# Kernel tuning notes

Measured on AMD Instinct MI355X. Metric: run time of the kernel, lower is better.

The kernel has to match this reference:

```python
import jax, jax.numpy as jnp
import numpy as np

H = 1024          # hidden_size
NH = 16           # num_heads = hidden_size // head_dim
DK = 64           # head_dim (key)
DV = 64           # head_v_dim
VDIM = 1024       # value_dim
DECAY_LR, GATE_LR, A_LR, V_LR = 64, 160, 64, 64
W_SCALE = -0.6065306597126334  # -exp(-0.5)
GN_EPS = 64 * 1e-5             # head_dim * norm_eps


def _lora(x, A, B, b, act):
    h = x @ A.T
    if act is not None:
        h = act(h)
    y = h @ B.T
    return y if b is None else y + b


def setup_inputs() -> dict:
    key = jax.random.key(0)
    ks = iter(jax.random.split(key, 40))
    def n(shape, s=0.02):
        return jax.random.normal(next(ks), shape, dtype=jnp.float32) * s
    inp = {
        'hidden_states': jax.random.normal(next(ks), (8, 2048, H), jnp.float32),
        'v_first': jax.random.normal(next(ks), (8, 2048, VDIM), jnp.float32),
        'x_r': n((1, 1, H), 0.5), 'x_w': n((1, 1, H), 0.5), 'x_k': n((1, 1, H), 0.5),
        'x_v': n((1, 1, H), 0.5), 'x_a': n((1, 1, H), 0.5), 'x_g': n((1, 1, H), 0.5),
        'k_k': 0.71 + n((H,), 0.05),
        'k_a': 1.02 + n((H,), 0.05),
        'r_k': -0.04 + n((NH, DK), 0.05),
        'W_r': n((H, H)), 'W_k': n((H, H)), 'W_v': n((VDIM, H)), 'W_o': n((H, VDIM)),
        'w_lora_A': n((DECAY_LR, H)), 'w_lora_B': n((H, DECAY_LR)), 'w_lora_b': n((H,), 0.5) - 4.0,
        'a_lora_A': n((A_LR, H)), 'a_lora_B': n((H, A_LR)), 'a_lora_b': n((H,), 0.1),
        'v_lora_A': n((V_LR, H)), 'v_lora_B': n((VDIM, V_LR)), 'v_lora_b': 0.73 + n((VDIM,), 0.1),
        'g_lora_A': n((GATE_LR, H)), 'g_lora_B': n((VDIM, GATE_LR)),
        'gn_w': jnp.ones((VDIM,), jnp.float32), 'gn_b': jnp.zeros((VDIM,), jnp.float32),
    }
    return inp


def reference(hidden_states, v_first, x_r, x_w, x_k, x_v, x_a, x_g, k_k, k_a, r_k,
              W_r, W_k, W_v, W_o, w_lora_A, w_lora_B, w_lora_b,
              a_lora_A, a_lora_B, a_lora_b, v_lora_A, v_lora_B, v_lora_b,
              g_lora_A, g_lora_B, gn_w, gn_b):
    x = hidden_states
    B_, T, _ = x.shape
    # token shift: delta[t] = x[t-1] - x[t], x[-1] = 0
    shifted = jnp.pad(x, ((0, 0), (1, 0), (0, 0)))[:, :T]
    delta = shifted - x
    xr = x + delta * x_r; xw = x + delta * x_w; xk = x + delta * x_k
    xv = x + delta * x_v; xa = x + delta * x_a; xg = x + delta * x_g

    r = xr @ W_r.T
    w = W_SCALE * jax.nn.sigmoid(_lora(xw, w_lora_A, w_lora_B, w_lora_b, jnp.tanh))  # log-decay in (-e^-0.5, 0)
    k = xk @ W_k.T
    v = xv @ W_v.T
    v = v + (v_first - v) * jax.nn.sigmoid(_lora(xv, v_lora_A, v_lora_B, v_lora_b, None))  # layer_idx != 0
    a = jax.nn.sigmoid(_lora(xa, a_lora_A, a_lora_B, a_lora_b, None))
    g = _lora(xg, g_lora_A, g_lora_B, None, jax.nn.sigmoid)

    kk = (k * k_k).reshape(B_, T, NH, DK)
    kk = kk / jnp.maximum(jnp.linalg.norm(kk, axis=-1, keepdims=True), 1e-12)  # l2 norm per head
    k = k * (1.0 + (a - 1.0) * k_a)

    rh = r.reshape(B_, T, NH, DK)
    wh = w.reshape(B_, T, NH, DK)
    kh = k.reshape(B_, T, NH, DK)
    vh = v.reshape(B_, T, NH, DV)
    ah = -kk                               # delta-rule 'a' (removal direction)
    bh = kk * a.reshape(B_, T, NH, DK)     # delta-rule 'b' (write direction)

    def step(S, inputs):
        # S: [B, H, DK, DV]; inputs each [B, H, D]
        r_t, w_t, k_t, v_t, a_t, b_t = inputs
        sa = jnp.einsum('bhk,bhkv->bhv', a_t, S)
        S = S * jnp.exp(w_t)[..., None] \
            + jnp.einsum('bhk,bhv->bhkv', b_t, sa) \
            + jnp.einsum('bhk,bhv->bhkv', k_t, v_t)
        o_t = jnp.einsum('bhk,bhkv->bhv', r_t, S)
        return S, o_t

    seq = tuple(jnp.moveaxis(t, 1, 0) for t in (rh, wh, kh, vh, ah, bh))  # [T,B,H,D]
    S0 = jnp.zeros((B_, NH, DK, DV), dtype=x.dtype)
    _, o = jax.lax.scan(step, S0, seq)
    o = jnp.moveaxis(o, 0, 1)  # [B, T, NH, DV]

    # GroupNorm with num_groups = num_heads over value_dim channels == per-head LayerNorm (no per-head affine)
    mu = o.mean(-1, keepdims=True)
    var = o.var(-1, keepdims=True)
    on = ((o - mu) / jnp.sqrt(var + GN_EPS)).reshape(B_, T, VDIM) * gn_w + gn_b

    bonus = ((rh * kh * r_k).sum(-1, keepdims=True) * vh).reshape(B_, T, VDIM)
    out = ((on + bonus) * g) @ W_o.T
    return out
```

## Files before the change

kernel.cpp:

```cpp
#include <hip/hip_runtime.h>
#include <hip/hip_bf16.h>


#define DEVI __device__ __forceinline__

constexpr int TSEQ = 2048;
constexpr int HID  = 1024;
constexpr int BTOT = 16384;
constexpr int CCH  = 32;
constexpr int NCH  = TSEQ / CCH;
constexpr int L4N  = 352;
constexpr float W_SCALE = -0.6065306597126334f;
constexpr float GN_EPS  = 6.4e-4f;

using s16x8  = __attribute__((ext_vector_type(8))) short;
using f32x4v = __attribute__((ext_vector_type(4))) float;

DEVI float4 ld4(const float* p) { return *reinterpret_cast<const float4*>(p); }
DEVI void   st4(float* p, float4 v) { *reinterpret_cast<float4*>(p) = v; }
DEVI float  sigf(float x) { return 1.0f / (1.0f + __expf(-x)); }
DEVI unsigned short bfr(float f) {
    unsigned int u = __float_as_uint(f);
    return (unsigned short)((u + 0x7fffu + ((u >> 16) & 1u)) >> 16);
}
DEVI float bff(unsigned short s) { return __uint_as_float(((unsigned int)s) << 16); }
DEVI unsigned int pk2(float lo, float hi) {
    return ((unsigned int)bfr(hi) << 16) | (unsigned int)bfr(lo);
}
DEVI void up8(uint4 u, float* f) {
    f[0]=bff((unsigned short)(u.x & 0xffffu)); f[1]=bff((unsigned short)(u.x >> 16));
    f[2]=bff((unsigned short)(u.y & 0xffffu)); f[3]=bff((unsigned short)(u.y >> 16));
    f[4]=bff((unsigned short)(u.z & 0xffffu)); f[5]=bff((unsigned short)(u.z >> 16));
    f[6]=bff((unsigned short)(u.w & 0xffffu)); f[7]=bff((unsigned short)(u.w >> 16));
}
DEVI f32x4v MF(s16x8 a, s16x8 b, f32x4v c) {
    return __builtin_amdgcn_mfma_f32_16x16x32_bf16(a, b, c, 0, 0, 0);
}
DEVI void gl16(const void* g, void* l) {
    __builtin_amdgcn_global_load_lds(
        (const __attribute__((address_space(1))) unsigned int*)g,
        (__attribute__((address_space(3))) unsigned int*)l, 16, 0, 0);
}
DEVI void gl4(const void* g, void* l) {
    __builtin_amdgcn_global_load_lds(
        (const __attribute__((address_space(1))) unsigned int*)g,
        (__attribute__((address_space(3))) unsigned int*)l, 4, 0, 0);
}

struct CastArgs {
    const float* src[12];
    unsigned short* dst[12];
    int start4[13];
};
__global__ __launch_bounds__(256) void cast_all_kernel(CastArgs a) {
    int i4 = blockIdx.x * 256 + threadIdx.x;
    if (i4 >= a.start4[12]) return;
    int seg = 0;
#pragma unroll
    for (int s = 1; s < 12; s++) seg += (i4 >= a.start4[s]) ? 1 : 0;
    int off = (i4 - a.start4[seg]) * 4;
    float4 v = ld4(a.src[seg] + off);
    ushort4 o; o.x = bfr(v.x); o.y = bfr(v.y); o.z = bfr(v.z); o.w = bfr(v.w);
    *reinterpret_cast<ushort4*>(a.dst[seg] + off) = o;
}

__global__ __launch_bounds__(256) void proj3_kernel(
        const float* __restrict__ x,
        const float* __restrict__ cr, const float* __restrict__ ck,
        const float* __restrict__ cv,
        const unsigned short* __restrict__ Wr, const unsigned short* __restrict__ Wk,
        const unsigned short* __restrict__ Wv,
        unsigned short* __restrict__ Ro, unsigned short* __restrict__ Ko,
        unsigned short* __restrict__ Vo) {
    __shared__ __align__(16) unsigned short As[3][64 * 32];
    __shared__ __align__(16) unsigned short Bs[3][128 * 32];
    const int tid = threadIdx.x;
    const int w = tid >> 6, l = tid & 63;
    const int bm = blockIdx.x * 64, bn = blockIdx.y * 128;
    const int wm = w >> 1, wn = w & 1;
    const int lr = l & 15, lq = l >> 4, lk = lq * 8;

    f32x4v acc[3][2][4];
#pragma unroll
    for (int p = 0; p < 3; p++)
#pragma unroll
        for (int i = 0; i < 2; i++)
#pragma unroll
            for (int j = 0; j < 4; j++)
#pragma unroll
                for (int q = 0; q < 4; q++) acc[p][i][j][q] = 0.f;

    const float* cvs[3] = {cr, ck, cv};
    const unsigned short* Ws[3] = {Wr, Wk, Wv};

    for (int k0 = 0; k0 < HID; k0 += 32) {
        {
            const int row = tid >> 2, kp = (tid & 3) * 8;
            const int gr = bm + row;
            const float* xp = x + (size_t)gr * HID + k0 + kp;
            float4 x0 = ld4(xp), x1 = ld4(xp + 4);
            float4 p0 = make_float4(0.f, 0.f, 0.f, 0.f), p1 = p0;
            if ((gr & (TSEQ - 1)) != 0) { p0 = ld4(xp - HID); p1 = ld4(xp - HID + 4); }
            float xb[8] = {x0.x, x0.y, x0.z, x0.w, x1.x, x1.y, x1.z, x1.w};
            float dx[8] = {p0.x - x0.x, p0.y - x0.y, p0.z - x0.z, p0.w - x0.w,
                           p1.x - x1.x, p1.y - x1.y, p1.z - x1.z, p1.w - x1.w};
#pragma unroll
            for (int p = 0; p < 3; p++) {
                float4 c0 = ld4(cvs[p] + k0 + kp), c1 = ld4(cvs[p] + k0 + kp + 4);
                float cc[8] = {c0.x, c0.y, c0.z, c0.w, c1.x, c1.y, c1.z, c1.w};
                uint4 u;
                u.x = pk2(fmaf(dx[0], cc[0], xb[0]), fmaf(dx[1], cc[1], xb[1]));
                u.y = pk2(fmaf(dx[2], cc[2], xb[2]), fmaf(dx[3], cc[3], xb[3]));
                u.z = pk2(fmaf(dx[4], cc[4], xb[4]), fmaf(dx[5], cc[5], xb[5]));
                u.w = pk2(fmaf(dx[6], cc[6], xb[6]), fmaf(dx[7], cc[7], xb[7]));
                *reinterpret_cast<uint4*>(&As[p][row * 32 + kp]) = u;
            }
        }
#pragma unroll
        for (int p = 0; p < 3; p++)
#pragma unroll
            for (int c = 0; c < 2; c++) {
                int idx = c * 256 + tid;
                int rw = idx >> 2, kp2 = (idx & 3) * 8;
                gl16(Ws[p] + (size_t)(bn + rw) * HID + k0 + kp2,
                     &Bs[p][c * 2048 + w * 512]);
            }
        __syncthreads();
#pragma unroll
        for (int p = 0; p < 3; p++) {
            s16x8 af[2], bf4[4];
#pragma unroll
            for (int i = 0; i < 2; i++)
                af[i] = *reinterpret_cast<const s16x8*>(
                    &As[p][(wm * 32 + i * 16 + lr) * 32 + lk]);
#pragma unroll
            for (int j = 0; j < 4; j++)
                bf4[j] = *reinterpret_cast<const s16x8*>(
                    &Bs[p][(wn * 64 + j * 16 + lr) * 32 + lk]);
#pragma unroll
            for (int i = 0; i < 2; i++)
#pragma unroll
                for (int j = 0; j < 4; j++)
                    acc[p][i][j] = MF(af[i], bf4[j], acc[p][i][j]);
        }
        __syncthreads();
    }

    unsigned short* dsts[3] = {Ro, Ko, Vo};
#pragma unroll
    for (int p = 0; p < 3; p++)
#pragma unroll
        for (int i = 0; i < 2; i++)
#pragma unroll
            for (int j = 0; j < 4; j++)
#pragma unroll
                for (int q = 0; q < 4; q++) {
                    const int grow = bm + wm * 32 + i * 16 + lq * 4 + q;
                    const int gcol = bn + wn * 64 + j * 16 + lr;
                    dsts[p][(size_t)grow * HID + gcol] = bfr(acc[p][i][j][q]);
                }
}

__global__ __launch_bounds__(256) void lora4_kernel(
        const float* __restrict__ x,
        const float* __restrict__ cv_, const float* __restrict__ cw_,
        const float* __restrict__ ca_, const float* __restrict__ cg_,
        const unsigned short* __restrict__ LW, unsigned short* __restrict__ H1) {
    __shared__ __align__(16) unsigned short As[4][64 * 32];
    __shared__ __align__(16) unsigned short Bs[L4N * 32];
    const int tid = threadIdx.x;
    const int w = tid >> 6, l = tid & 63;
    const int lr = l & 15, lq = l >> 4, lk = lq * 8;
    const int bm = blockIdx.x * 64;
    const float* cvs[4] = {cv_, cw_, ca_, cg_};

    f32x4v acc[22];
#pragma unroll
    for (int j = 0; j < 22; j++)
#pragma unroll
        for (int q = 0; q < 4; q++) acc[j][q] = 0.f;

    for (int k0 = 0; k0 < HID; k0 += 32) {
        {
            const int row = tid >> 2, kp = (tid & 3) * 8;
            const int gr = bm + row;
            const float* xp = x + (size_t)gr * HID + k0 + kp;
            float4 x0 = ld4(xp), x1 = ld4(xp + 4);
            float4 p0 = make_float4(0.f, 0.f, 0.f, 0.f), p1 = p0;
            if ((gr & (TSEQ - 1)) != 0) { p0 = ld4(xp - HID); p1 = ld4(xp - HID + 4); }
            float xb[8] = {x0.x, x0.y, x0.z, x0.w, x1.x, x1.y, x1.z, x1.w};
            float dx[8] = {p0.x - x0.x, p0.y - x0.y, p0.z - x0.z, p0.w - x0.w,
                           p1.x - x1.x, p1.y - x1.y, p1.z - x1.z, p1.w - x1.w};
#pragma unroll
            for (int p = 0; p < 4; p++) {
                float4 c0 = ld4(cvs[p] + k0 + kp), c1 = ld4(cvs[p] + k0 + kp + 4);
                float cc[8] = {c0.x, c0.y, c0.z, c0.w, c1.x, c1.y, c1.z, c1.w};
                uint4 u;
                u.x = pk2(fmaf(dx[0], cc[0], xb[0]), fmaf(dx[1], cc[1], xb[1]));
                u.y = pk2(fmaf(dx[2], cc[2], xb[2]), fmaf(dx[3], cc[3], xb[3]));
                u.z = pk2(fmaf(dx[4], cc[4], xb[4]), fmaf(dx[5], cc[5], xb[5]));
                u.w = pk2(fmaf(dx[6], cc[6], xb[6]), fmaf(dx[7], cc[7], xb[7]));
                *reinterpret_cast<uint4*>(&As[p][row * 32 + kp]) = u;
            }
        }
#pragma unroll
        for (int c = 0; c < 6; c++) {
            int idx = c * 256 + tid;
            if (idx < L4N * 4) {
                gl16(LW + (size_t)(idx >> 2) * HID + (idx & 3) * 8 + k0,
                     (char*)&Bs[0] + (c * 256 + w * 64) * 16);
            }
        }
        __syncthreads();
        s16x8 af[4];
#pragma unroll
        for (int p = 0; p < 4; p++)
            af[p] = *reinterpret_cast<const s16x8*>(&As[p][(w * 16 + lr) * 32 + lk]);
#pragma unroll
        for (int j = 0; j < 22; j++) {
            const int grp = (j < 4) ? 0 : (j < 8) ? 1 : (j < 12) ? 2 : 3;
            s16x8 bf = *reinterpret_cast<const s16x8*>(&Bs[(j * 16 + lr) * 32 + lk]);
            acc[j] = MF(af[grp], bf, acc[j]);
        }
        __syncthreads();
    }

#pragma unroll
    for (int j = 0; j < 22; j++)
#pragma unroll
        for (int q = 0; q < 4; q++) {
            const int grow = bm + w * 16 + lq * 4 + q;
            const int gcol = j * 16 + lr;
            float d = acc[j][q];
            if (j >= 4 && j < 8) d = tanhf(d);
            else if (j >= 12) d = sigf(d);
            H1[(size_t)grow * L4N + gcol] = bfr(d);
        }
}

__global__ __launch_bounds__(256) void stage2_kernel(
        const unsigned short* __restrict__ H1,
        const unsigned short* __restrict__ vB16, const unsigned short* __restrict__ wB16,
        const unsigned short* __restrict__ aB16,
        const float* __restrict__ vb, const float* __restrict__ wb,
        const float* __restrict__ ab,
        unsigned short* __restrict__ Vout, unsigned short* __restrict__ Wout,
        unsigned short* __restrict__ Aout,
        const unsigned short* __restrict__ aux1, const float* __restrict__ aux2) {
    const int z = blockIdx.z;
    const unsigned short* Bw = (z == 0) ? vB16 : (z == 1) ? wB16 : aB16;
    const float* bias = (z == 0) ? vb : (z == 1) ? wb : ab;
    unsigned short* Cout = (z == 0) ? Vout : (z == 1) ? Wout : Aout;
    const int aoff = z * 64;
    __shared__ __align__(16) unsigned short As[128 * 32];
    __shared__ __align__(16) unsigned short Bs[128 * 32];
    const int tid = threadIdx.x;
    const int w = tid >> 6, l = tid & 63;
    const int bm = blockIdx.x * 128, bn = blockIdx.y * 128;
    const int wm = w >> 1, wn = w & 1;
    const int lr = l & 15, lk = (l >> 4) * 8;

    f32x4v acc[4][4];
#pragma unroll
    for (int i = 0; i < 4; i++)
#pragma unroll
        for (int j = 0; j < 4; j++)
#pragma unroll
            for (int q = 0; q < 4; q++) acc[i][j][q] = 0.f;

    for (int k0 = 0; k0 < 64; k0 += 32) {
#pragma unroll
        for (int c = 0; c < 2; c++) {
            int idx = c * 256 + tid;
            int row = idx >> 2, kp = (idx & 3) * 8;
            gl16(H1 + (size_t)(bm + row) * L4N + aoff + k0 + kp,
                 &As[c * 2048 + w * 512]);
        }
#pragma unroll
        for (int c = 0; c < 2; c++) {
            int idx = c * 256 + tid;
            int row = idx >> 2, kp = (idx & 3) * 8;
            gl16(Bw + (size_t)(bn + row) * 64 + k0 + kp, &Bs[c * 2048 + w * 512]);
        }
        __syncthreads();
        s16x8 afx[4], bfx[4];
#pragma unroll
        for (int i = 0; i < 4; i++)
            afx[i] = *reinterpret_cast<const s16x8*>(&As[(wm * 64 + i * 16 + lr) * 32 + lk]);
#pragma unroll
        for (int j = 0; j < 4; j++)
            bfx[j] = *reinterpret_cast<const s16x8*>(&Bs[(wn * 64 + j * 16 + lr) * 32 + lk]);
#pragma unroll
        for (int i = 0; i < 4; i++)
#pragma unroll
            for (int j = 0; j < 4; j++)
                acc[i][j] = MF(afx[i], bfx[j], acc[i][j]);
        __syncthreads();
    }

#pragma unroll
    for (int i = 0; i < 4; i++) {
        const int grow0 = bm + wm * 64 + i * 16 + (l >> 4) * 4;
#pragma unroll
        for (int j = 0; j < 4; j++) {
            const int gcol = bn + wn * 64 + j * 16 + lr;
            const float bsv = bias[gcol];
#pragma unroll
            for (int q = 0; q < 4; q++) {
                const int grow = grow0 + q;
                float d = acc[i][j][q];
                if (z == 0) {
                    float v0 = bff(aux1[(size_t)grow * HID + gcol]);
                    d = fmaf(aux2[(size_t)grow * HID + gcol] - v0, sigf(d + bsv), v0);
                } else if (z == 1) {
                    d = W_SCALE * sigf(d + bsv);
                } else {
                    d = sigf(d + bsv);
                }
                Cout[(size_t)grow * HID + gcol] = bfr(d);
            }
        }
    }
}

template<int BM, int BN, int MODE, bool OUTBF>
__global__ __launch_bounds__(256) void mgemm(
        const unsigned short* __restrict__ Ab, const unsigned short* __restrict__ Bw,
        void* Cout, int N, int K, int lda,
        const float* __restrict__ bias,
        const unsigned short* aux1, const float* __restrict__ aux2) {
    constexpr int BK = 32;
    constexpr int WM_ = (BN == 128) ? 2 : 4;
    constexpr int WN_ = (BN == 128) ? 2 : 1;
    constexpr int WTM = BM / WM_, WTN = BN / WN_;
    constexpr int MF_ = WTM / 16, NF = WTN / 16;
    constexpr int ACALLS = (BM * BK) / 2048;
    constexpr int BCALLS = (BN * BK) / 2048;
    __shared__ __align__(16) unsigned short As[BM * BK];
    __shared__ __align__(16) unsigned short Bs[BN * BK];
    const int tid = threadIdx.x;
    const int w = tid >> 6, l = tid & 63;
    const int bm = blockIdx.x * BM, bn = blockIdx.y * BN;
    const int wm = w / WN_, wn = w % WN_;
    const int lr = l & 15, lk = (l >> 4) * 8;

    f32x4v acc[MF_][NF];
#pragma unroll
    for (int i = 0; i < MF_; i++)
#pragma unroll
        for (int j = 0; j < NF; j++)
#pragma unroll
            for (int q = 0; q < 4; q++) acc[i][j][q] = 0.f;

    for (int k0 = 0; k0 < K; k0 += BK) {
#pragma unroll
        for (int c = 0; c < ACALLS; c++) {
            int idx = c * 256 + tid;
            int row = idx >> 2, kp = (idx & 3) * 8;
            gl16(Ab + (size_t)(bm + row) * lda + k0 + kp, &As[c * 2048 + w * 512]);
        }
#pragma unroll
        for (int c = 0; c < BCALLS; c++) {
            int idx = c * 256 + tid;
            int row = idx >> 2, kp = (idx & 3) * 8;
            int gc = bn + row; if (gc > N - 1) gc = N - 1;
            gl16(Bw + (size_t)gc * K + k0 + kp, &Bs[c * 2048 + w * 512]);
        }
        __syncthreads();
        s16x8 afx[MF_], bfx[NF];
#pragma unroll
        for (int i = 0; i < MF_; i++)
            afx[i] = *reinterpret_cast<const s16x8*>(&As[(wm * WTM + i * 16 + lr) * BK + lk]);
#pragma unroll
        for (int j = 0; j < NF; j++)
            bfx[j] = *reinterpret_cast<const s16x8*>(&Bs[(wn * WTN + j * 16 + lr) * BK + lk]);
#pragma unroll
        for (int i = 0; i < MF_; i++)
#pragma unroll
            for (int j = 0; j < NF; j++)
                acc[i][j] = __builtin_amdgcn_mfma_f32_16x16x32_bf16(
                    afx[i], bfx[j], acc[i][j], 0, 0, 0);
        __syncthreads();
    }

#pragma unroll
    for (int i = 0; i < MF_; i++) {
        const int grow0 = bm + wm * WTM + i * 16 + (l >> 4) * 4;
#pragma unroll
        for (int j = 0; j < NF; j++) {
            const int gcol = bn + wn * WTN + j * 16 + lr;
            if (gcol >= N) continue;
#pragma unroll
            for (int q = 0; q < 4; q++) {
                const int grow = grow0 + q;
                float d = acc[i][j][q];
                if (OUTBF) ((unsigned short*)Cout)[(size_t)grow * N + gcol] = bfr(d);
                else       ((float*)Cout)[(size_t)grow * N + gcol] = d;
            }
        }
    }
}

__global__ __launch_bounds__(64) void cprep_kernel(
        unsigned short* __restrict__ K16, unsigned short* __restrict__ A16,
        unsigned short* __restrict__ R16, unsigned short* __restrict__ KK16,
        const unsigned short* __restrict__ W16,
        const float* __restrict__ kkc, const float* __restrict__ kac,
        const float* __restrict__ rkw,
        float* __restrict__ SB, float* __restrict__ Ed,
        unsigned short* __restrict__ MvH, unsigned short* __restrict__ MvL) {
    __shared__ __align__(16) unsigned short sA[32][64], sB[32][64];
    __shared__ __align__(16) float Mab[32][36];
    const int bid = blockIdx.x;
    const int bh = bid >> 6, ch = bid & 63;
    const int bb = bh >> 4, hh = bh & 15;
    const int l = threadIdx.x;
    const int chn = hh * 64 + l;
    const float kkcv = kkc[chn], kacv = kac[chn], rkv = rkw[chn];
    size_t off = ((size_t)(bb * TSEQ) + ch * CCH) * HID + chn;
    float cw = 0.f, er = 1.f;
    for (int i = 0; i < CCH; i++, off += HID) {
        const float k = bff(K16[off]);
        const float a = bff(A16[off]);
        const float r = bff(R16[off]);
        const float wv = bff(W16[off]);
        const float kr = k * kkcv;
        float ss = kr * kr;
        ss += __shfl_xor(ss, 1);  ss += __shfl_xor(ss, 2);
        ss += __shfl_xor(ss, 4);  ss += __shfl_xor(ss, 8);
        ss += __shfl_xor(ss, 16); ss += __shfl_xor(ss, 32);
        const float inv = 1.0f / fmaxf(sqrtf(ss), 1e-12f);
        const float kk = kr * inv;
        const float b  = kk * a;
        const float kn = k * fmaf(a - 1.0f, kacv, 1.0f);
        float s3 = r * kn * rkv;
        s3 += __shfl_xor(s3, 1);  s3 += __shfl_xor(s3, 2);
        s3 += __shfl_xor(s3, 4);  s3 += __shfl_xor(s3, 8);
        s3 += __shfl_xor(s3, 16); s3 += __shfl_xor(s3, 32);
        if (l == 0) SB[(size_t)bh * TSEQ + ch * CCH + i] = s3;
        const float cwp = cw; cw += wv;
        const float ea = __expf(cwp), ei = __expf(-cw);
        er = __expf(cw);
        const unsigned short At = bfr(-kk * ea);
        const unsigned short Bt = bfr(b * ei);
        KK16[off] = At;
        A16[off]  = Bt;
        K16[off]  = bfr(kn * ei);
        R16[off]  = bfr(r * er);
        sA[i][l] = At; sB[i][l] = Bt;
    }
    Ed[((size_t)bh * NCH + ch) * 64 + l] = er;
    __syncthreads();
    const int lr = l & 15, lq = l >> 4;
    f32x4v z4; z4[0] = z4[1] = z4[2] = z4[3] = 0.f;
#pragma unroll
    for (int mi = 0; mi < 2; mi++)
#pragma unroll
        for (int ni = 0; ni < 2; ni++) {
            s16x8 a0 = *reinterpret_cast<const s16x8*>(&sA[mi * 16 + lr][lq * 8]);
            s16x8 a1 = *reinterpret_cast<const s16x8*>(&sA[mi * 16 + lr][32 + lq * 8]);
            s16x8 b0 = *reinterpret_cast<const s16x8*>(&sB[ni * 16 + lr][lq * 8]);
            s16x8 b1 = *reinterpret_cast<const s16x8*>(&sB[ni * 16 + lr][32 + lq * 8]);
            f32x4v m = MF(a1, b1, MF(a0, b0, z4));
#pragma unroll
            for (int q = 0; q < 4; q++) {
                int r = mi * 16 + lq * 4 + q, cc2 = ni * 16 + lr;
                Mab[r][cc2] = (cc2 < r) ? m[q] : 0.f;
            }
        }
    __syncthreads();
    const int j = l & 31;
    float m[32];
#pragma unroll
    for (int i = 0; i < 32; i++) m[i] = (i == j) ? 1.f : 0.f;
#pragma unroll
    for (int i = 1; i < 32; i++) {
        float p0 = 0.f, p1 = 0.f, p2 = 0.f, p3 = 0.f;
#pragma unroll
        for (int k4_ = 0; k4_ < 32; k4_ += 4) {
            if (k4_ >= i) break;
            float4 L4 = *reinterpret_cast<const float4*>(&Mab[i][k4_]);
            p0 = fmaf(L4.x, m[k4_ + 0], p0);
            if (k4_ + 1 < i) p1 = fmaf(L4.y, m[k4_ + 1], p1);
            if (k4_ + 2 < i) p2 = fmaf(L4.z, m[k4_ + 2], p2);
            if (k4_ + 3 < i) p3 = fmaf(L4.w, m[k4_ + 3], p3);
        }
        m[i] += (p0 + p1) + (p2 + p3);
    }
    if (l < 32) {
        unsigned short* dH = MvH + (size_t)(bh * NCH + ch) * 1024;
        unsigned short* dL = MvL + (size_t)(bh * NCH + ch) * 1024;
#pragma unroll
        for (int i = 0; i < 32; i++) {
            unsigned short h = bfr(m[i]);
            dH[i * 32 + j] = h;
            dL[i * 32 + j] = bfr(m[i] - bff(h));
        }
    }
}

__global__ __launch_bounds__(256) void recchunk_kernel(
        const unsigned short* __restrict__ AtG, const unsigned short* __restrict__ BtG,
        const unsigned short* __restrict__ KtG, const unsigned short* __restrict__ RtG,
        const unsigned short* __restrict__ V16, const float* __restrict__ Ed,
        const unsigned short* __restrict__ MvH, const unsigned short* __restrict__ MvL,
        unsigned short* __restrict__ Ob16) {
    __shared__ __align__(16) unsigned short stT[2][4][CCH][64];
    __shared__ __align__(16) unsigned short stMh[2][32][32], stMl[2][32][32];
    __shared__ __align__(16) unsigned short stV[2][CCH][16];
    __shared__ __align__(16) float stEd[2][64];
    __shared__ __align__(16) unsigned short Shi[16][74], Slo[16][74];
    __shared__ __align__(16) unsigned short BtT[64][42], KtT[64][42];
    __shared__ __align__(16) unsigned short VT[16][42];
    __shared__ __align__(16) unsigned short MakH[32][42], MakL[32][42];
    __shared__ __align__(16) unsigned short MrkH[32][42], MrkL[32][42];
    __shared__ __align__(16) unsigned short MrbH[32][42], MrbL[32][42];
    __shared__ __align__(16) unsigned short rhTH[16][42], rhTL[16][42];

    const int bid = blockIdx.x;
    const int vq = bid >> 7, bh = bid & 127;
    const int tid = threadIdx.x;
    const int w = tid >> 6, l = tid & 63;
    const int lr = l & 15, lq = l >> 4;
    const int bb = bh >> 4, hh = bh & 15;
    const size_t rowoff = ((size_t)bb * TSEQ) * HID + hh * 64;
    const int mi = w >> 1, ni = w & 1;

    const int r8 = l >> 3, ck = l & 7;
    const int swz8 = (ck ^ r8) * 8;

    auto STAGE = [&](int buf, int cn) {
        if (cn >= NCH) return;
        const size_t cb = rowoff + (size_t)(cn * CCH) * HID;
        const unsigned short* srcs[4] = {AtG, BtG, KtG, RtG};
        const unsigned short* T = srcs[w];
#pragma unroll
        for (int c = 0; c < 4; c++)
            gl16(T + cb + (size_t)(c * 8 + r8) * HID + swz8, &stT[buf][w][c * 8][0]);
        if (w == 0) {
            gl16(V16 + cb + (size_t)(l >> 1) * HID + vq * 16 + (l & 1) * 8,
                 &stV[buf][0][0]);
            gl4(Ed + ((size_t)bh * NCH + cn) * 64 + l, &stEd[buf][0]);
        } else if (w == 1) {
#pragma unroll
            for (int c = 0; c < 2; c++)
                gl16(MvH + (size_t)(bh * NCH + cn) * 1024 + c * 512 + l * 8,
                     (char*)&stMh[buf][0][0] + c * 1024);
        } else if (w == 2) {
#pragma unroll
            for (int c = 0; c < 2; c++)
                gl16(MvL + (size_t)(bh * NCH + cn) * 1024 + c * 512 + l * 8,
                     (char*)&stMl[buf][0][0] + c * 1024);
        }
    };

    for (int idx = tid; idx < 16 * 74; idx += 256) {
        ((unsigned short*)Shi)[idx] = 0;
        ((unsigned short*)Slo)[idx] = 0;
    }
    STAGE(0, 0);
    asm volatile("s_waitcnt vmcnt(0)" ::: "memory");
    __syncthreads();

    auto fragT = [&](int bf, int tn, int rbase, int kb) -> s16x8 {
        int row = rbase + lr;
        int chv = ((kb >> 3) + lq) ^ (row & 7);
        return *reinterpret_cast<const s16x8*>(
            (const char*)&stT[bf][tn][0][0] + row * 128 + chv * 16);
    };
    auto fragS = [&](const unsigned short (*Sx)[74], int kb) -> s16x8 {
        return *reinterpret_cast<const s16x8*>(&Sx[lr][kb + lq * 8]);
    };
    auto frag42 = [&](const unsigned short (*T)[42], int rbase) -> s16x8 {
        return *reinterpret_cast<const s16x8*>(&T[rbase + lr][lq * 8]);
    };

    f32x4v Sacc;
#pragma unroll
    for (int q = 0; q < 4; q++) Sacc[q] = 0.f;
    f32x4v z4; z4[0] = z4[1] = z4[2] = z4[3] = 0.f;

    int buf = 0;
    for (int c = 0; c < NCH; c++) {
        STAGE(buf ^ 1, c + 1);
        {
            const int tt = tid & 31, g8 = tid >> 5;
            const int ch = g8 ^ (tt & 7);
            uint4 bu = *reinterpret_cast<const uint4*>(&stT[buf][1][tt][ch * 8]);
            uint4 ku = *reinterpret_cast<const uint4*>(&stT[buf][2][tt][ch * 8]);
            unsigned int bw[4] = {bu.x, bu.y, bu.z, bu.w};
            unsigned int kw[4] = {ku.x, ku.y, ku.z, ku.w};
#pragma unroll
            for (int e = 0; e < 4; e++) {
                BtT[g8 * 8 + 2 * e][tt]     = (unsigned short)(bw[e] & 0xffffu);
                BtT[g8 * 8 + 2 * e + 1][tt] = (unsigned short)(bw[e] >> 16);
                KtT[g8 * 8 + 2 * e][tt]     = (unsigned short)(kw[e] & 0xffffu);
                KtT[g8 * 8 + 2 * e + 1][tt] = (unsigned short)(kw[e] >> 16);
            }
            if (g8 < 4) {
                ushort4 vu = *reinterpret_cast<const ushort4*>(&stV[buf][tt][g8 * 4]);
                VT[g8 * 4 + 0][tt] = vu.x; VT[g8 * 4 + 1][tt] = vu.y;
                VT[g8 * 4 + 2][tt] = vu.z; VT[g8 * 4 + 3][tt] = vu.w;
            }
        }
        s16x8 atm0 = fragT(buf, 0, mi * 16, 0), atm1 = fragT(buf, 0, mi * 16, 32);
        s16x8 rt0  = fragT(buf, 3, mi * 16, 0), rt1  = fragT(buf, 3, mi * 16, 32);
        s16x8 bt0  = fragT(buf, 1, ni * 16, 0), bt1  = fragT(buf, 1, ni * 16, 32);
        s16x8 kt0  = fragT(buf, 2, ni * 16, 0), kt1  = fragT(buf, 2, ni * 16, 32);
        f32x4v mak = MF(atm1, kt1, MF(atm0, kt0, z4));
        f32x4v mrk = MF(rt1, kt1, MF(rt0, kt0, z4));
        f32x4v mrb = MF(rt1, bt1, MF(rt0, bt0, z4));
        f32x4v oac = z4, rhT = z4;
        {
            s16x8 sh0 = fragS(Shi, 0), sh1 = fragS(Shi, 32);
            s16x8 sl0 = fragS(Slo, 0), sl1 = fragS(Slo, 32);
            if (ni == 0) {
                oac = MF(rt1, sl1, MF(rt0, sl0, MF(rt1, sh1, MF(rt0, sh0, z4))));
            } else {
                rhT = MF(sl1, atm1, MF(sl0, atm0, MF(sh1, atm1, MF(sh0, atm0, z4))));
            }
        }
#pragma unroll
        for (int q = 0; q < 4; q++) {
            const int r = mi * 16 + lq * 4 + q, cc = ni * 16 + lr;
            float vv = (cc < r) ? mak[q] : 0.f;
            unsigned short h = bfr(vv);
            MakH[r][cc] = h; MakL[r][cc] = bfr(vv - bff(h));
            vv = (cc <= r) ? mrk[q] : 0.f; h = bfr(vv);
            MrkH[r][cc] = h; MrkL[r][cc] = bfr(vv - bff(h));
            vv = (cc <= r) ? mrb[q] : 0.f; h = bfr(vv);
            MrbH[r][cc] = h; MrbL[r][cc] = bfr(vv - bff(h));
        }
        __syncthreads();
        {
            s16x8 vt0 = frag42(VT, 0);
            if (ni == 0) {
                oac = MF(frag42(MrkL, mi * 16), vt0,
                         MF(frag42(MrkH, mi * 16), vt0, oac));
            } else {
                rhT = MF(vt0, frag42(MakL, mi * 16),
                         MF(vt0, frag42(MakH, mi * 16), rhT));
#pragma unroll
                for (int q = 0; q < 4; q++) {
                    const int r = lq * 4 + q, cc = mi * 16 + lr;
                    unsigned short h = bfr(rhT[q]);
                    rhTH[r][cc] = h; rhTL[r][cc] = bfr(rhT[q] - bff(h));
                }
            }
        }
        __syncthreads();
        if (ni == 1) {
            s16x8 rh0 = frag42(rhTH, 0), rl0 = frag42(rhTL, 0);
            s16x8 mvh = *reinterpret_cast<const s16x8*>(&stMh[buf][mi * 16 + lr][lq * 8]);
            s16x8 mvl = *reinterpret_cast<const s16x8*>(&stMl[buf][mi * 16 + lr][lq * 8]);
            f32x4v sat = MF(rl0, mvh, MF(rh0, mvl, MF(rh0, mvh, z4)));
#pragma unroll
            for (int q = 0; q < 4; q++) {
                const int r = lq * 4 + q, cc = mi * 16 + lr;
                unsigned short h = bfr(sat[q]);
                MakH[r][cc] = h;
                MakL[r][cc] = bfr(sat[q] - bff(h));
            }
        }
        __syncthreads();
        {
            s16x8 sath = frag42(MakH, 0), satl = frag42(MakL, 0);
            if (ni == 0) {
                s16x8 rbh = frag42(MrbH, mi * 16), rbl = frag42(MrbL, mi * 16);
                oac = MF(rbl, sath, MF(rbh, satl, MF(rbh, sath, oac)));
#pragma unroll
                for (int q = 0; q < 4; q++) {
                    const int t = c * CCH + mi * 16 + lq * 4 + q;
                    Ob16[rowoff + (size_t)t * HID + vq * 16 + lr] = bfr(oac[q]);
                }
            }
            s16x8 btf = frag42(BtT, w * 16);
            s16x8 ktf = frag42(KtT, w * 16);
            s16x8 vta = frag42(VT, 0);
            const float ed = stEd[buf][w * 16 + lr];
            Sacc = MF(sath, btf, Sacc);
            Sacc = MF(satl, btf, Sacc);
            Sacc = MF(vta, ktf, Sacc);
#pragma unroll
            for (int q = 0; q < 4; q++) {
                Sacc[q] *= ed;
                unsigned short h = bfr(Sacc[q]);
                Shi[lq * 4 + q][w * 16 + lr] = h;
                Slo[lq * 4 + q][w * 16 + lr] = bfr(Sacc[q] - bff(h));
            }
        }
        asm volatile("s_waitcnt vmcnt(0)" ::: "memory");
        __syncthreads();
        buf ^= 1;
    }
}

__global__ __launch_bounds__(256) void stats_kernel(
        const unsigned short* __restrict__ O16, float* __restrict__ MS) {
    const int row = blockIdx.x;
    const int tid = threadIdx.x;
    const int c = tid * 4;
    ushort4 ou = *reinterpret_cast<const ushort4*>(O16 + (size_t)row * HID + c);
    float o[4] = {bff(ou.x), bff(ou.y), bff(ou.z), bff(ou.w)};
    float s1 = o[0] + o[1] + o[2] + o[3];
    float s2 = o[0]*o[0] + o[1]*o[1] + o[2]*o[2] + o[3]*o[3];
#pragma unroll
    for (int m = 1; m < 16; m <<= 1) {
        s1 += __shfl_xor(s1, m); s2 += __shfl_xor(s2, m);
    }
    if ((tid & 15) == 0) {
        const int hh = tid >> 4;
        const float mu = s1 * (1.0f / 64.0f);
        const float var = s2 * (1.0f / 64.0f) - mu * mu;
        float2 v; v.x = mu; v.y = rsqrtf(var + GN_EPS);
        *reinterpret_cast<float2*>(MS + (size_t)row * 32 + hh * 2) = v;
    }
}

__global__ __launch_bounds__(256) void wogemm_kernel(
        const unsigned short* __restrict__ O16, const unsigned short* __restrict__ V16,
        const unsigned short* __restrict__ G16, const float* __restrict__ SB,
        const float* __restrict__ MS, const float* __restrict__ gnw,
        const float* __restrict__ gnb, const unsigned short* __restrict__ Wo,
        float* __restrict__ out) {
    __shared__ __align__(16) unsigned short As[128 * 32];
    __shared__ __align__(16) unsigned short Bs[128 * 32];
    const int tid = threadIdx.x;
    const int w = tid >> 6, l = tid & 63;
    const int bm = blockIdx.x * 128, bn = blockIdx.y * 128;
    const int wm = w >> 1, wn = w & 1;
    const int lr = l & 15, lk = (l >> 4) * 8;

    f32x4v acc[4][4];
#pragma unroll
    for (int i = 0; i < 4; i++)
#pragma unroll
        for (int j = 0; j < 4; j++)
#pragma unroll
            for (int q = 0; q < 4; q++) acc[i][j][q] = 0.f;

    for (int k0 = 0; k0 < HID; k0 += 32) {
#pragma unroll
        for (int c = 0; c < 2; c++) {
            int idx = c * 256 + tid;
            int row = idx >> 2, kp = (idx & 3) * 8;
            const int gr = bm + row;
            const size_t rb = (size_t)gr * HID + k0 + kp;
            uint4 ou = *reinterpret_cast<const uint4*>(O16 + rb);
            uint4 vu = *reinterpret_cast<const uint4*>(V16 + rb);
            uint4 gu = *reinterpret_cast<const uint4*>(G16 + rb);
            float o8[8], v8[8], g8[8];
            up8(ou, o8); up8(vu, v8); up8(gu, g8);
            const int hh = (k0 + kp) >> 6;
            float2 ms = *reinterpret_cast<const float2*>(MS + (size_t)gr * 32 + hh * 2);
            const float s3 = SB[((size_t)(gr >> 11) * 16 + hh) * TSEQ + (gr & (TSEQ - 1))];
            float4 w0 = ld4(gnw + k0 + kp), w1 = ld4(gnw + k0 + kp + 4);
            float4 b0 = ld4(gnb + k0 + kp), b1 = ld4(gnb + k0 + kp + 4);
            float wn8[8] = {w0.x, w0.y, w0.z, w0.w, w1.x, w1.y, w1.z, w1.w};
            float bn8[8] = {b0.x, b0.y, b0.z, b0.w, b1.x, b1.y, b1.z, b1.w};
            float y[8];
#pragma unroll
            for (int e = 0; e < 8; e++)
                y[e] = (fmaf((o8[e] - ms.x) * ms.y, wn8[e], bn8[e]) + s3 * v8[e]) * g8[e];
            uint4 u;
            u.x = pk2(y[0], y[1]); u.y = pk2(y[2], y[3]);
            u.z = pk2(y[4], y[5]); u.w = pk2(y[6], y[7]);
            *reinterpret_cast<uint4*>(&As[idx * 8]) = u;
        }
#pragma unroll
        for (int c = 0; c < 2; c++) {
            int idx = c * 256 + tid;
            int row = idx >> 2, kp = (idx & 3) * 8;
            gl16(Wo + (size_t)(bn + row) * HID + k0 + kp, &Bs[c * 2048 + w * 512]);
        }
        __syncthreads();
        s16x8 afx[4], bfx[4];
#pragma unroll
        for (int i = 0; i < 4; i++)
            afx[i] = *reinterpret_cast<const s16x8*>(&As[(wm * 64 + i * 16 + lr) * 32 + lk]);
#pragma unroll
        for (int j = 0; j < 4; j++)
            bfx[j] = *reinterpret_cast<const s16x8*>(&Bs[(wn * 64 + j * 16 + lr) * 32 + lk]);
#pragma unroll
        for (int i = 0; i < 4; i++)
#pragma unroll
            for (int j = 0; j < 4; j++)
                acc[i][j] = MF(afx[i], bfx[j], acc[i][j]);
        __syncthreads();
    }

#pragma unroll
    for (int i = 0; i < 4; i++) {
        const int grow0 = bm + wm * 64 + i * 16 + (l >> 4) * 4;
#pragma unroll
        for (int j = 0; j < 4; j++) {
            const int gcol = bn + wn * 64 + j * 16 + lr;
#pragma unroll
            for (int q = 0; q < 4; q++)
                out[(size_t)(grow0 + q) * HID + gcol] = acc[i][j][q];
        }
    }
}

extern "C" void kernel_launch(void* const* d_in, const int* in_sizes, int n_in,
                              void* d_out, int out_size, void* d_ws, size_t ws_size,
                              hipStream_t stream) {
    const float* x   = (const float*)d_in[0];
    const float* vf  = (const float*)d_in[1];
    const float* x_r = (const float*)d_in[2];
    const float* x_w = (const float*)d_in[3];
    const float* x_k = (const float*)d_in[4];
    const float* x_v = (const float*)d_in[5];
    const float* x_a = (const float*)d_in[6];
    const float* x_g = (const float*)d_in[7];
    const float* k_k = (const float*)d_in[8];
    const float* k_a = (const float*)d_in[9];
    const float* r_k = (const float*)d_in[10];
    const float* W_r = (const float*)d_in[11];
    const float* W_k = (const float*)d_in[12];
    const float* W_v = (const float*)d_in[13];
    const float* W_o = (const float*)d_in[14];
    const float* wA  = (const float*)d_in[15];
    const float* wB  = (const float*)d_in[16];
    const float* wb  = (const float*)d_in[17];
    const float* aA  = (const float*)d_in[18];
    const float* aB  = (const float*)d_in[19];
    const float* ab  = (const float*)d_in[20];
    const float* vA  = (const float*)d_in[21];
    const float* vB  = (const float*)d_in[22];
    const float* vb  = (const float*)d_in[23];
    const float* gA  = (const float*)d_in[24];
    const float* gB  = (const float*)d_in[25];
    const float* gnw = (const float*)d_in[26];
    const float* gnb = (const float*)d_in[27];
    float* out = (float*)d_out;

    float* ws = (float*)d_ws;
    const size_t SZ = (size_t)BTOT * HID;
    const size_t HH = (size_t)HID * HID;
    float*          REG  = ws;
    unsigned short* P    = (unsigned short*)(ws + SZ);
    unsigned short* R16  = P;
    unsigned short* K16  = P + 1 * SZ;
    unsigned short* V16  = P + 2 * SZ;
    unsigned short* A16  = P + 3 * SZ;
    unsigned short* KK16 = P + 4 * SZ;
    unsigned short* H1   = P + 5 * SZ;
    unsigned short* WR   = H1 + (size_t)BTOT * L4N;
    unsigned short* Wr16 = WR;
    unsigned short* Wk16 = WR + 1 * HH;
    unsigned short* Wv16 = WR + 2 * HH;
    unsigned short* Wo16 = WR + 3 * HH;
    unsigned short* LW   = WR + 4 * HH;
    unsigned short* vB16 = LW + (size_t)L4N * HID;
    unsigned short* wB16 = vB16 + 65536;
    unsigned short* aB16 = wB16 + 65536;
    unsigned short* gB16 = aB16 + 65536;
    float*          SB   = (float*)(gB16 + 163840);
    float*          Ed   = SB + (size_t)128 * TSEQ;
    float*          MS   = Ed;
    unsigned short* W16   = (unsigned short*)REG;
    unsigned short* O16   = (unsigned short*)REG;
    unsigned short* MinvH = (unsigned short*)(REG + 8 * 1024 * 1024);
    unsigned short* MinvL = MinvH + (size_t)128 * NCH * 1024;
    unsigned short* G16   = (unsigned short*)(REG + 8 * 1024 * 1024);

    const dim3 blk(256);
    const dim3 gBig(128, 8);
    const dim3 gP3(BTOT / 64, 8);
    const unsigned short* nu = nullptr;
    const float* np = nullptr;

    CastArgs ca;
    const float* srcs[12] = {W_r, W_k, W_v, W_o, vA, wA, aA, gA, vB, wB, aB, gB};
    unsigned short* dsts[12] = {Wr16, Wk16, Wv16, Wo16,
                                LW, LW + 65536, LW + 131072, LW + 196608,
                                vB16, wB16, aB16, gB16};
    int cnts[12] = {(int)HH, (int)HH, (int)HH, (int)HH,
                    65536, 65536, 65536, 163840, 65536, 65536, 65536, 163840};
    int acc4 = 0;
    for (int s = 0; s < 12; s++) {
        ca.src[s] = srcs[s]; ca.dst[s] = dsts[s];
        ca.start4[s] = acc4;
        acc4 += cnts[s] / 4;
    }
    ca.start4[12] = acc4;
    cast_all_kernel<<<dim3((acc4 + 255) / 256), blk, 0, stream>>>(ca);

    proj3_kernel<<<gP3, blk, 0, stream>>>(
        x, x_r, x_k, x_v, Wr16, Wk16, Wv16, R16, K16, V16);
    lora4_kernel<<<dim3(BTOT / 64), blk, 0, stream>>>(
        x, x_v, x_w, x_a, x_g, LW, H1);
    stage2_kernel<<<dim3(128, 8, 3), blk, 0, stream>>>(
        H1, vB16, wB16, aB16, vb, wb, ab, V16, W16, A16, V16, vf);
    cprep_kernel<<<dim3(128 * NCH), dim3(64), 0, stream>>>(
        K16, A16, R16, KK16, W16, k_k, k_a, r_k, SB, Ed, MinvH, MinvL);
    recchunk_kernel<<<dim3(512), blk, 0, stream>>>(
        KK16, A16, K16, R16, V16, Ed, MinvH, MinvL, O16);
    mgemm<128,128,0,true><<<gBig, blk, 0, stream>>>(
        H1 + 192, gB16, G16, HID, 160, L4N, np, nu, np);
    stats_kernel<<<dim3(BTOT), blk, 0, stream>>>(O16, MS);
    wogemm_kernel<<<gBig, blk, 0, stream>>>(
        O16, V16, G16, SB, MS, gnw, gnb, Wo16, out);
    (void)in_sizes; (void)n_in; (void)out_size; (void)ws_size;
}
```

Before: 1.045 ms.

## Precompute Minv·Mak and Minv·At in cprep to shorten recchunk chain

Moves the per-chunk products that recchunk recomputed for every value slice into cprep. cprep now builds the Mak matrix and multiplies the inverted triangular matrix by Mak (stored as hi/lo bf16) and by At (stored in KK16). recchunk loads these premultiplied operands, which removes one dependent matmul stage and one block barrier per chunk and redistributes work across warps. In exchange cprep does extra scalar FMA work with LDS-heavy loops, and the reassociation may change rounding.

```diff
diff --git a/kernel.cpp b/kernel.cpp
--- a/kernel.cpp
+++ b/kernel.cpp
@@ -409,15 +409,16 @@
         const float* __restrict__ rkw,
         float* __restrict__ SB, float* __restrict__ Ed,
         unsigned short* __restrict__ MvH, unsigned short* __restrict__ MvL) {
-    __shared__ __align__(16) unsigned short sA[32][64], sB[32][64];
-    __shared__ __align__(16) float Mab[32][36];
+    __shared__ __align__(16) unsigned short sA[32][64], sB[32][64], sK[32][64];
+    __shared__ __align__(16) float Mab[32][36], Mak[32][36], Mnv[32][36];
     const int bid = blockIdx.x;
     const int bh = bid >> 6, ch = bid & 63;
     const int bb = bh >> 4, hh = bh & 15;
     const int l = threadIdx.x;
     const int chn = hh * 64 + l;
     const float kkcv = kkc[chn], kacv = kac[chn], rkv = rkw[chn];
-    size_t off = ((size_t)(bb * TSEQ) + ch * CCH) * HID + chn;
+    const size_t off0 = ((size_t)(bb * TSEQ) + ch * CCH) * HID + chn;
+    size_t off = off0;
     float cw = 0.f, er = 1.f;
     for (int i = 0; i < CCH; i++, off += HID) {
         const float k = bff(K16[off]);
@@ -443,11 +444,11 @@
         er = __expf(cw);
         const unsigned short At = bfr(-kk * ea);
         const unsigned short Bt = bfr(b * ei);
-        KK16[off] = At;
-        A16[off]  = Bt;
-        K16[off]  = bfr(kn * ei);
-        R16[off]  = bfr(r * er);
-        sA[i][l] = At; sB[i][l] = Bt;
+        const unsigned short Kt = bfr(kn * ei);
+        A16[off] = Bt;
+        K16[off] = Kt;
+        R16[off] = bfr(r * er);
+        sA[i][l] = At; sB[i][l] = Bt; sK[i][l] = Kt;
     }
     Ed[((size_t)bh * NCH + ch) * 64 + l] = er;
     __syncthreads();
@@ -461,11 +462,15 @@
             s16x8 a1 = *reinterpret_cast<const s16x8*>(&sA[mi * 16 + lr][32 + lq * 8]);
             s16x8 b0 = *reinterpret_cast<const s16x8*>(&sB[ni * 16 + lr][lq * 8]);
             s16x8 b1 = *reinterpret_cast<const s16x8*>(&sB[ni * 16 + lr][32 + lq * 8]);
-            f32x4v m = MF(a1, b1, MF(a0, b0, z4));
+            s16x8 k0 = *reinterpret_cast<const s16x8*>(&sK[ni * 16 + lr][lq * 8]);
+            s16x8 k1 = *reinterpret_cast<const s16x8*>(&sK[ni * 16 + lr][32 + lq * 8]);
+            f32x4v m  = MF(a1, b1, MF(a0, b0, z4));
+            f32x4v mk = MF(a1, k1, MF(a0, k0, z4));
 #pragma unroll
             for (int q = 0; q < 4; q++) {
                 int r = mi * 16 + lq * 4 + q, cc2 = ni * 16 + lr;
                 Mab[r][cc2] = (cc2 < r) ? m[q] : 0.f;
+                Mak[r][cc2] = (cc2 < r) ? mk[q] : 0.f;
             }
         }
     __syncthreads();
@@ -488,22 +493,40 @@
         m[i] += (p0 + p1) + (p2 + p3);
     }
     if (l < 32) {
+#pragma unroll
+        for (int i = 0; i < 32; i++) Mnv[i][j] = m[i];
+    }
+    __syncthreads();
+    {
         unsigned short* dH = MvH + (size_t)(bh * NCH + ch) * 1024;
         unsigned short* dL = MvL + (size_t)(bh * NCH + ch) * 1024;
-#pragma unroll
-        for (int i = 0; i < 32; i++) {
-            unsigned short h = bfr(m[i]);
-            dH[i * 32 + j] = h;
-            dL[i * 32 + j] = bfr(m[i] - bff(h));
+        const int tp = l & 31;
+        const int th = (l >> 5) * 16;
+        for (int t = 0; t < 16; t++) {
+            float s = 0.f;
+#pragma unroll 8
+            for (int jj = 0; jj < 32; jj++) s = fmaf(Mnv[th + t][jj], Mak[jj][tp], s);
+            unsigned short h = bfr(s);
+            dH[(th + t) * 32 + tp] = h;
+            dL[(th + t) * 32 + tp] = bfr(s - bff(h));
+        }
+    }
+    {
+        size_t offr = off0;
+        for (int t = 0; t < 32; t++, offr += HID) {
+            float s = 0.f;
+#pragma unroll 8
+            for (int jj = 0; jj < 32; jj++) s = fmaf(Mnv[t][jj], bff(sA[jj][l]), s);
+            KK16[offr] = bfr(s);
         }
     }
 }
 
 __global__ __launch_bounds__(256) void recchunk_kernel(
-        const unsigned short* __restrict__ AtG, const unsigned short* __restrict__ BtG,
+        const unsigned short* __restrict__ AMG, const unsigned short* __restrict__ BtG,
         const unsigned short* __restrict__ KtG, const unsigned short* __restrict__ RtG,
         const unsigned short* __restrict__ V16, const float* __restrict__ Ed,
-        const unsigned short* __restrict__ MvH, const unsigned short* __restrict__ MvL,
+        const unsigned short* __restrict__ LMH, const unsigned short* __restrict__ LML,
         unsigned short* __restrict__ Ob16) {
     __shared__ __align__(16) unsigned short stT[2][4][CCH][64];
     __shared__ __align__(16) unsigned short stMh[2][32][32], stMl[2][32][32];
@@ -512,10 +535,9 @@
     __shared__ __align__(16) unsigned short Shi[16][74], Slo[16][74];
     __shared__ __align__(16) unsigned short BtT[64][42], KtT[64][42];
     __shared__ __align__(16) unsigned short VT[16][42];
-    __shared__ __align__(16) unsigned short MakH[32][42], MakL[32][42];
     __shared__ __align__(16) unsigned short MrkH[32][42], MrkL[32][42];
     __shared__ __align__(16) unsigned short MrbH[32][42], MrbL[32][42];
-    __shared__ __align__(16) unsigned short rhTH[16][42], rhTL[16][42];
+    __shared__ __align__(16) unsigned short SATh[16][42], SATl[16][42];
 
     const int bid = blockIdx.x;
     const int vq = bid >> 7, bh = bid & 127;
@@ -532,7 +554,7 @@
     auto STAGE = [&](int buf, int cn) {
         if (cn >= NCH) return;
         const size_t cb = rowoff + (size_t)(cn * CCH) * HID;
-        const unsigned short* srcs[4] = {AtG, BtG, KtG, RtG};
+        const unsigned short* srcs[4] = {AMG, BtG, KtG, RtG};
         const unsigned short* T = srcs[w];
 #pragma unroll
         for (int c = 0; c < 4; c++)
@@ -544,12 +566,12 @@
         } else if (w == 1) {
 #pragma unroll
             for (int c = 0; c < 2; c++)
-                gl16(MvH + (size_t)(bh * NCH + cn) * 1024 + c * 512 + l * 8,
+                gl16(LMH + (size_t)(bh * NCH + cn) * 1024 + c * 512 + l * 8,
                      (char*)&stMh[buf][0][0] + c * 1024);
         } else if (w == 2) {
 #pragma unroll
             for (int c = 0; c < 2; c++)
-                gl16(MvL + (size_t)(bh * NCH + cn) * 1024 + c * 512 + l * 8,
+                gl16(LML + (size_t)(bh * NCH + cn) * 1024 + c * 512 + l * 8,
                      (char*)&stMl[buf][0][0] + c * 1024);
         }
     };
@@ -603,77 +625,62 @@
                 VT[g8 * 4 + 2][tt] = vu.z; VT[g8 * 4 + 3][tt] = vu.w;
             }
         }
-        s16x8 atm0 = fragT(buf, 0, mi * 16, 0), atm1 = fragT(buf, 0, mi * 16, 32);
-        s16x8 rt0  = fragT(buf, 3, mi * 16, 0), rt1  = fragT(buf, 3, mi * 16, 32);
-        s16x8 bt0  = fragT(buf, 1, ni * 16, 0), bt1  = fragT(buf, 1, ni * 16, 32);
-        s16x8 kt0  = fragT(buf, 2, ni * 16, 0), kt1  = fragT(buf, 2, ni * 16, 32);
-        f32x4v mak = MF(atm1, kt1, MF(atm0, kt0, z4));
-        f32x4v mrk = MF(rt1, kt1, MF(rt0, kt0, z4));
-        f32x4v mrb = MF(rt1, bt1, MF(rt0, bt0, z4));
-        f32x4v oac = z4, rhT = z4;
-        {
+        __syncthreads();
+        f32x4v oac = z4;
+        if (ni == 0) {
+            s16x8 rt0 = fragT(buf, 3, mi * 16, 0), rt1 = fragT(buf, 3, mi * 16, 32);
             s16x8 sh0 = fragS(Shi, 0), sh1 = fragS(Shi, 32);
             s16x8 sl0 = fragS(Slo, 0), sl1 = fragS(Slo, 32);
-            if (ni == 0) {
-                oac = MF(rt1, sl1, MF(rt0, sl0, MF(rt1, sh1, MF(rt0, sh0, z4))));
-            } else {
-                rhT = MF(sl1, atm1, MF(sl0, atm0, MF(sh1, atm1, MF(sh0, atm0, z4))));
-            }
-        }
-#pragma unroll
-        for (int q = 0; q < 4; q++) {
-            const int r = mi * 16 + lq * 4 + q, cc = ni * 16 + lr;
-            float vv = (cc < r) ? mak[q] : 0.f;
-            unsigned short h = bfr(vv);
-            MakH[r][cc] = h; MakL[r][cc] = bfr(vv - bff(h));
-            vv = (cc <= r) ? mrk[q] : 0.f; h = bfr(vv);
-            MrkH[r][cc] = h; MrkL[r][cc] = bfr(vv - bff(h));
-            vv = (cc <= r) ? mrb[q] : 0.f; h = bfr(vv);
-            MrbH[r][cc] = h; MrbL[r][cc] = bfr(vv - bff(h));
-        }
-        __syncthreads();
-        {
+            oac = MF(rt1, sl1, MF(rt0, sl0, MF(rt1, sh1, MF(rt0, sh0, z4))));
+#pragma unroll
+            for (int n = 0; n < 2; n++) {
+                s16x8 kt0 = fragT(buf, 2, n * 16, 0), kt1 = fragT(buf, 2, n * 16, 32);
+                s16x8 bt0 = fragT(buf, 1, n * 16, 0), bt1 = fragT(buf, 1, n * 16, 32);
+                f32x4v mrk = MF(rt1, kt1, MF(rt0, kt0, z4));
+                f32x4v mrb = MF(rt1, bt1, MF(rt0, bt0, z4));
+#pragma unroll
+                for (int q = 0; q < 4; q++) {
+                    const int r = mi * 16 + lq * 4 + q, cc = n * 16 + lr;
+                    float vv = (cc <= r) ? mrk[q] : 0.f;
+                    unsigned short h = bfr(vv);
+                    MrkH[r][cc] = h; MrkL[r][cc] = bfr(vv - bff(h));
+                    vv = (cc <= r) ? mrb[q] : 0.f; h = bfr(vv);
+                    MrbH[r][cc] = h; MrbL[r][cc] = bfr(vv - bff(h));
+                }
+            }
+        } else {
+            s16x8 am0 = fragT(buf, 0, mi * 16, 0), am1 = fragT(buf, 0, mi * 16, 32);
+            s16x8 sh0 = fragS(Shi, 0), sh1 = fragS(Shi, 32);
+            s16x8 sl0 = fragS(Slo, 0), sl1 = fragS(Slo, 32);
             s16x8 vt0 = frag42(VT, 0);
-            if (ni == 0) {
-                oac = MF(frag42(MrkL, mi * 16), vt0,
-                         MF(frag42(MrkH, mi * 16), vt0, oac));
-            } else {
-                rhT = MF(vt0, frag42(MakL, mi * 16),
-                         MF(vt0, frag42(MakH, mi * 16), rhT));
-#pragma unroll
-                for (int q = 0; q < 4; q++) {
-                    const int r = lq * 4 + q, cc = mi * 16 + lr;
-                    unsigned short h = bfr(rhT[q]);
-                    rhTH[r][cc] = h; rhTL[r][cc] = bfr(rhT[q] - bff(h));
-                }
-            }
-        }
-        __syncthreads();
-        if (ni == 1) {
-            s16x8 rh0 = frag42(rhTH, 0), rl0 = frag42(rhTL, 0);
-            s16x8 mvh = *reinterpret_cast<const s16x8*>(&stMh[buf][mi * 16 + lr][lq * 8]);
-            s16x8 mvl = *reinterpret_cast<const s16x8*>(&stMl[buf][mi * 16 + lr][lq * 8]);
-            f32x4v sat = MF(rl0, mvh, MF(rh0, mvl, MF(rh0, mvh, z4)));
+            s16x8 lmh = *reinterpret_cast<const s16x8*>(&stMh[buf][mi * 16 + lr][lq * 8]);
+            s16x8 lml = *reinterpret_cast<const s16x8*>(&stMl[buf][mi * 16 + lr][lq * 8]);
+            f32x4v sat = MF(sl1, am1, MF(sl0, am0, MF(sh1, am1, MF(sh0, am0, z4))));
+            sat = MF(vt0, lml, MF(vt0, lmh, sat));
 #pragma unroll
             for (int q = 0; q < 4; q++) {
                 const int r = lq * 4 + q, cc = mi * 16 + lr;
                 unsigned short h = bfr(sat[q]);
-                MakH[r][cc] = h;
-                MakL[r][cc] = bfr(sat[q] - bff(h));
-            }
-        }
-        __syncthreads();
+                SATh[r][cc] = h;
+                SATl[r][cc] = bfr(sat[q] - bff(h));
+            }
+        }
+        __syncthreads();
+        if (ni == 0) {
+            s16x8 vt0 = frag42(VT, 0);
+            oac = MF(frag42(MrkL, mi * 16), vt0,
+                     MF(frag42(MrkH, mi * 16), vt0, oac));
+            s16x8 sath = frag42(SATh, 0), satl = frag42(SATl, 0);
+            s16x8 rbh = frag42(MrbH, mi * 16), rbl = frag42(MrbL, mi * 16);
+            oac = MF(rbl, sath, MF(rbh, satl, MF(rbh, sath, oac)));
+#pragma unroll
+            for (int q = 0; q < 4; q++) {
+                const int t = c * CCH + mi * 16 + lq * 4 + q;
+                Ob16[rowoff + (size_t)t * HID + vq * 16 + lr] = bfr(oac[q]);
+            }
+        }
         {
-            s16x8 sath = frag42(MakH, 0), satl = frag42(MakL, 0);
-            if (ni == 0) {
-                s16x8 rbh = frag42(MrbH, mi * 16), rbl = frag42(MrbL, mi * 16);
-                oac = MF(rbl, sath, MF(rbh, satl, MF(rbh, sath, oac)));
-#pragma unroll
-                for (int q = 0; q < 4; q++) {
-                    const int t = c * CCH + mi * 16 + lq * 4 + q;
-                    Ob16[rowoff + (size_t)t * HID + vq * 16 + lr] = bfr(oac[q]);
-                }
-            }
+            s16x8 sath = frag42(SATh, 0), satl = frag42(SATl, 0);
             s16x8 btf = frag42(BtT, w * 16);
             s16x8 ktf = frag42(KtT, w * 16);
             s16x8 vta = frag42(VT, 0);
@@ -861,8 +868,8 @@
     float*          MS   = Ed;
     unsigned short* W16   = (unsigned short*)REG;
     unsigned short* O16   = (unsigned short*)REG;
-    unsigned short* MinvH = (unsigned short*)(REG + 8 * 1024 * 1024);
-    unsigned short* MinvL = MinvH + (size_t)128 * NCH * 1024;
+    unsigned short* LMHp  = (unsigned short*)(REG + 8 * 1024 * 1024);
+    unsigned short* LMLp  = LMHp + (size_t)128 * NCH * 1024;
     unsigned short* G16   = (unsigned short*)(REG + 8 * 1024 * 1024);
 
     const dim3 blk(256);
@@ -894,9 +901,9 @@
     stage2_kernel<<<dim3(128, 8, 3), blk, 0, stream>>>(
         H1, vB16, wB16, aB16, vb, wb, ab, V16, W16, A16, V16, vf);
     cprep_kernel<<<dim3(128 * NCH), dim3(64), 0, stream>>>(
-        K16, A16, R16, KK16, W16, k_k, k_a, r_k, SB, Ed, MinvH, MinvL);
+        K16, A16, R16, KK16, W16, k_k, k_a, r_k, SB, Ed, LMHp, LMLp);
     recchunk_kernel<<<dim3(512), blk, 0, stream>>>(
-        KK16, A16, K16, R16, V16, Ed, MinvH, MinvL, O16);
+        KK16, A16, K16, R16, V16, Ed, LMHp, LMLp, O16);
     mgemm<128,128,0,true><<<gBig, blk, 0, stream>>>(
         H1 + 192, gB16, G16, HID, 160, L4N, np, nu, np);
     stats_kernel<<<dim3(BTOT), blk, 0, stream>>>(O16, MS);
```

Measured after the change: 1.206 ms. 15.4% more time.
